# Optimization experiments

Measured on AMD Instinct MI355X. Metric: run time of the kernel, lower is better.

## Reference

```python
import jax, jax.numpy as jnp
import numpy as np

B, T, C, H = 8, 1024, 1024, 16
D = C // H
EPS = 1e-5

def _ln(x, g, b):
    mu = jnp.mean(x, axis=-1, keepdims=True)
    var = jnp.var(x, axis=-1, keepdims=True)
    return (x - mu) * jax.lax.rsqrt(var + EPS) * g + b

def _build_mask(cond_mask, cond_len, token_len):
    # Vectorized form of the per-batch Python-loop mask in the torch module.
    counts = jnp.sum(cond_mask, axis=-1)            # [B] number of valid cond tokens
    rows = jnp.arange(T)
    cols = jnp.arange(T)
    # all rows may attend to the first counts[i] (cond) columns
    m_cond = cols[None, None, :] < counts[:, None, None]          # [B,1,T]
    m_cond = jnp.broadcast_to(m_cond, (B, T, T))
    # block-causal tiled pattern on rows/cols >= cond_len:
    # value = (col - cond_len) % token_len <= (row - cond_len) % token_len
    pattern = ((cols[None, :] - cond_len) % token_len) <= ((rows[:, None] - cond_len) % token_len)
    m_block = (rows[:, None] >= cond_len) & (cols[None, :] >= cond_len) & pattern  # [T,T]
    # cols >= cond_len: overwritten by block pattern (rows < cond_len stay 0 there)
    mask = jnp.where(cols[None, None, :] < cond_len, m_cond, m_block[None, :, :])
    return mask[:, None, :, :]                      # [B,1,T,T] bool

def _attn(x, Wq, bq, Wk, bk, Wv, bv, Wp, bp, cond_mask, cond_len, token_len):
    q = (x @ Wq + bq).reshape(B, T, H, D).transpose(0, 2, 1, 3)  # [B,H,T,D]
    k = (x @ Wk + bk).reshape(B, T, H, D).transpose(0, 2, 1, 3)
    v = (x @ Wv + bv).reshape(B, T, H, D).transpose(0, 2, 1, 3)
    att = jnp.einsum('bhqd,bhkd->bhqk', q, k) * (1.0 / np.sqrt(D))
    mask = _build_mask(cond_mask, cond_len, token_len)
    att = jnp.where(mask, att, -jnp.inf)
    att = jax.nn.softmax(att, axis=-1)
    y = jnp.einsum('bhqk,bhkd->bhqd', att, v)
    y = y.transpose(0, 2, 1, 3).reshape(B, T, C)
    return y @ Wp + bp

def setup_inputs() -> dict:
    key = jax.random.key(0)
    ks = jax.random.split(key, 16)
    cond_len, token_len = 256, 768
    s = 1.0 / np.sqrt(C)
    counts = jax.random.randint(ks[0], (B,), 1, cond_len + 1)
    cond_mask = (jnp.arange(T)[None, :] < counts[:, None]).astype(jnp.int32)
    return {
        'x': jax.random.normal(ks[1], (B, T, C), jnp.float32),
        'ln1_g': jnp.ones((C,), jnp.float32), 'ln1_b': jnp.zeros((C,), jnp.float32),
        'Wq': jax.random.normal(ks[2], (C, C), jnp.float32) * s, 'bq': jnp.zeros((C,), jnp.float32),
        'Wk': jax.random.normal(ks[3], (C, C), jnp.float32) * s, 'bk': jnp.zeros((C,), jnp.float32),
        'Wv': jax.random.normal(ks[4], (C, C), jnp.float32) * s, 'bv': jnp.zeros((C,), jnp.float32),
        'Wp': jax.random.normal(ks[5], (C, C), jnp.float32) * s, 'bp': jnp.zeros((C,), jnp.float32),
        'ln2_g': jnp.ones((C,), jnp.float32), 'ln2_b': jnp.zeros((C,), jnp.float32),
        'W1': jax.random.normal(ks[6], (C, 4 * C), jnp.float32) * s, 'b1': jnp.zeros((4 * C,), jnp.float32),
        'W2': jax.random.normal(ks[7], (4 * C, C), jnp.float32) * (0.5 * s), 'b2': jnp.zeros((C,), jnp.float32),
        'cond_mask': cond_mask,
        'cond_len': cond_len,
        'token_len': token_len,
    }

def reference(x, ln1_g, ln1_b, Wq, bq, Wk, bk, Wv, bv, Wp, bp, ln2_g, ln2_b, W1, b1, W2, b2, cond_mask, cond_len, token_len):
    x = x + _attn(_ln(x, ln1_g, ln1_b), Wq, bq, Wk, bk, Wv, bv, Wp, bp, cond_mask, cond_len, token_len)
    h = _ln(x, ln2_g, ln2_b)
    x = x + (jax.nn.gelu(h @ W1 + b1, approximate=False) @ W2 + b2)
    return x
```

## Files before the change

kernel.cpp:

```cpp
#include <hip/hip_runtime.h>
#include <hip/hip_bf16.h>
#include <cstdint>
#include <cstddef>

typedef __attribute__((ext_vector_type(8))) short short8;
typedef __attribute__((ext_vector_type(4))) float f32x4;
typedef __attribute__((ext_vector_type(4))) unsigned short us4;

#define MFMA_BF16(a, b, c) __builtin_amdgcn_mfma_f32_16x16x32_bf16((a), (b), (c), 0, 0, 0)
#define VMCNT(n) asm volatile("s_waitcnt vmcnt(" #n ")" ::: "memory")

__device__ __forceinline__ unsigned short f2bf(float f) {
  unsigned int u = __float_as_uint(f);
  u += 0x7FFFu + ((u >> 16) & 1u);
  return (unsigned short)(u >> 16);
}

typedef const void __attribute__((address_space(1)))* as1_cvp;
typedef void __attribute__((address_space(3)))* as3_vp;
__device__ __forceinline__ void gll16(const short* g, short* l) {
#if defined(__HIP_DEVICE_COMPILE__)
  __builtin_amdgcn_global_load_lds((as1_cvp)g, (as3_vp)l, 16, 0, 0);
#else
  (void)g; (void)l;
#endif
}

__global__ void count_kernel(const int* __restrict__ cm, int* __restrict__ counts) {
  __shared__ int sd[256];
  const int b = blockIdx.x, t = threadIdx.x;
  int s = 0;
  for (int i = t; i < 1024; i += 256) s += cm[b * 1024 + i];
  sd[t] = s; __syncthreads();
  for (int k = 128; k > 0; k >>= 1) { if (t < k) sd[t] += sd[t + k]; __syncthreads(); }
  if (t == 0) counts[b] = sd[0];
}

__global__ void pack_bias_kernel(const float* __restrict__ bq, const float* __restrict__ bk,
                                 const float* __restrict__ bv, float* __restrict__ dst) {
  int i = blockIdx.x * 256 + threadIdx.x;
  dst[i] = (i < 1024) ? bq[i] : (i < 2048 ? bk[i - 1024] : bv[i - 2048]);
}

__global__ void transpose_kernel(const float* __restrict__ src, unsigned short* __restrict__ dst,
                                 int R, int C) {
  __shared__ float tile[32][33];
  const int c0 = blockIdx.x * 32, r0 = blockIdx.y * 32;
  const int tx = threadIdx.x, ty = threadIdx.y;
  #pragma unroll
  for (int i = ty; i < 32; i += 8)
    tile[i][tx] = src[(size_t)(r0 + i) * C + (c0 + tx)];
  __syncthreads();
  #pragma unroll
  for (int i = ty; i < 32; i += 8)
    dst[(size_t)(c0 + i) * R + (r0 + tx)] = f2bf(tile[tx][i]);
}

__global__ void vtrans_kernel(const short* __restrict__ qkv, short* __restrict__ vtr) {
  __shared__ short tile[32][33];
  const int bh = blockIdx.z;
  const int t0 = blockIdx.x * 32, d0 = blockIdx.y * 32;
  const int b = bh >> 4, h = bh & 15;
  const int tx = threadIdx.x, ty = threadIdx.y;
  const short* src = qkv + (size_t)b * 1024 * 3072 + 2048 + h * 64;
  #pragma unroll
  for (int i = ty; i < 32; i += 8)
    tile[i][tx] = src[(size_t)(t0 + i) * 3072 + d0 + tx];
  __syncthreads();
  short* dst = vtr + (size_t)bh * 65536;
  #pragma unroll
  for (int i = ty; i < 32; i += 8)
    dst[(d0 + i) * 1024 + t0 + tx] = tile[tx][i];
}

__global__ __launch_bounds__(256) void ln_kernel(const float* __restrict__ in,
                                                 const float* __restrict__ gw,
                                                 const float* __restrict__ bw,
                                                 unsigned short* __restrict__ out) {
  const int row = blockIdx.x, t = threadIdx.x;
  const float4 v = ((const float4*)(in + (size_t)row * 1024))[t];
  float s = v.x + v.y + v.z + v.w;
  float ss = v.x * v.x + v.y * v.y + v.z * v.z + v.w * v.w;
  #pragma unroll
  for (int o = 32; o >= 1; o >>= 1) { s += __shfl_down(s, o, 64); ss += __shfl_down(ss, o, 64); }
  __shared__ float red[8];
  if ((t & 63) == 0) { red[t >> 6] = s; red[4 + (t >> 6)] = ss; }
  __syncthreads();
  const float S  = red[0] + red[1] + red[2] + red[3];
  const float SS = red[4] + red[5] + red[6] + red[7];
  const float mu = S * (1.0f / 1024.0f);
  const float var = SS * (1.0f / 1024.0f) - mu * mu;
  const float rs = rsqrtf(var + 1e-5f);
  const int c = t * 4;
  const float4 g4 = ((const float4*)gw)[t];
  const float4 b4 = ((const float4*)bw)[t];
  us4 o4;
  o4[0] = f2bf((v.x - mu) * rs * g4.x + b4.x);
  o4[1] = f2bf((v.y - mu) * rs * g4.y + b4.y);
  o4[2] = f2bf((v.z - mu) * rs * g4.z + b4.z);
  o4[3] = f2bf((v.w - mu) * rs * g4.w + b4.w);
  *(us4*)(out + (size_t)row * 1024 + c) = o4;
}

template <int EPI>
__global__ __launch_bounds__(512, 1) void gemm_k2_kernel(
    const short* __restrict__ A, const short* __restrict__ BT,
    const float* __restrict__ bias, int N, int K, int gm,
    unsigned short* __restrict__ outb, float* __restrict__ outf,
    const float* __restrict__ res) {
  __shared__ alignas(16) short lds[73728];
  const int t = threadIdx.x;
  const int l = t & 63, w = t >> 6;
  const int lq = l & 15, g = l >> 4;
  const int wr = w >> 2, wc = w & 3;
  const int cpx = (int)gridDim.x >> 3;
  const int wid = ((int)blockIdx.x & 7) * cpx + ((int)blockIdx.x >> 3);
  const int bm = (wid % gm) * 256, bn = (wid / gm) * 128;
  const int NT = K >> 6;

  const int csw = ((t & 7) ^ ((t >> 3) & 7)) * 8;
  const int sA = t >> 3;
  const int sB = ((t >> 8) & 1) * 64 + ((t >> 3) & 31);

  const f32x4 z4 = {0.f, 0.f, 0.f, 0.f};
  f32x4 acc[8][2];
  #pragma unroll
  for (int i = 0; i < 8; i++) { acc[i][0] = z4; acc[i][1] = z4; }

  auto stageA = [&](int buf, int h, int k0) {
    const short* src = A + (size_t)(bm + h * 64 + sA) * K + k0 + csw;
    short* dst = lds + buf * 24576 + h * 8192 + t * 8;
    gll16(src, dst);
    gll16(src + (size_t)128 * K, dst + 4096);
  };
  auto stageB = [&](int buf, int h, int k0) {
    const short* src = BT + (size_t)(bn + h * 32 + sB) * K + k0 + csw;
    short* dst = lds + buf * 24576 + 16384 + h * 4096 + t * 8;
    gll16(src, dst);
  };
  auto rdA = [&](int buf, int mh, int mi2, int kk) {
    const int ra = wr * 64 + mi2 * 16 + lq;
    const int unit = (kk * 4 + g) ^ (ra & 7);
    return *(const short8*)(lds + buf * 24576 + mh * 8192 + ra * 64 + unit * 8);
  };
  auto rdB = [&](int buf, int ni2, int kk) {
    const int h = wc & 1;
    const int rb = (wc >> 1) * 32 + ni2 * 16 + lq;
    const int unit = (kk * 4 + g) ^ (rb & 7);
    return *(const short8*)(lds + buf * 24576 + 16384 + h * 4096 + rb * 64 + unit * 8);
  };

  stageA(0, 0, 0);  stageB(0, 0, 0);
  stageA(0, 1, 0);  stageB(0, 1, 0);
  stageA(1, 0, 64); stageB(1, 0, 64);
  VMCNT(3);
  __builtin_amdgcn_s_barrier();

  int cur = 0;
  for (int v = 0; v < NT; ++v) {
    const int nx1 = (cur == 2) ? 0 : cur + 1;
    const int nx2 = (nx1 == 2) ? 0 : nx1 + 1;
    short8 a[4][2], b[2][2], a2[4][2];
    #pragma unroll
    for (int mi2 = 0; mi2 < 4; ++mi2)
      #pragma unroll
      for (int kk = 0; kk < 2; ++kk) a[mi2][kk] = rdA(cur, 0, mi2, kk);
    #pragma unroll
    for (int ni2 = 0; ni2 < 2; ++ni2)
      #pragma unroll
      for (int kk = 0; kk < 2; ++kk) b[ni2][kk] = rdB(cur, ni2, kk);
    if (v + 1 < NT) { stageA(nx1, 1, (v + 1) * 64); stageB(nx1, 1, (v + 1) * 64); }
    __builtin_amdgcn_s_setprio(1);
    #pragma unroll
    for (int mi2 = 0; mi2 < 4; ++mi2)
      #pragma unroll
      for (int ni2 = 0; ni2 < 2; ++ni2)
        #pragma unroll
        for (int kk = 0; kk < 2; ++kk)
          acc[mi2][ni2] = MFMA_BF16(a[mi2][kk], b[ni2][kk], acc[mi2][ni2]);
    __builtin_amdgcn_s_setprio(0);
    #pragma unroll
    for (int mi2 = 0; mi2 < 4; ++mi2)
      #pragma unroll
      for (int kk = 0; kk < 2; ++kk) a2[mi2][kk] = rdA(cur, 1, mi2, kk);
    if (v + 2 < NT) {
      stageA(nx2, 0, (v + 2) * 64); stageB(nx2, 0, (v + 2) * 64);
      VMCNT(3);
    } else {
      VMCNT(0);
    }
    __builtin_amdgcn_s_barrier();
    __builtin_amdgcn_s_setprio(1);
    #pragma unroll
    for (int mi2 = 0; mi2 < 4; ++mi2)
      #pragma unroll
      for (int ni2 = 0; ni2 < 2; ++ni2)
        #pragma unroll
        for (int kk = 0; kk < 2; ++kk)
          acc[4 + mi2][ni2] = MFMA_BF16(a2[mi2][kk], b[ni2][kk], acc[4 + mi2][ni2]);
    __builtin_amdgcn_s_setprio(0);
    cur = nx1;
  }

  if (EPI == 2) {
    #pragma unroll
    for (int mi = 0; mi < 8; ++mi) {
      #pragma unroll
      for (int ni = 0; ni < 2; ++ni) {
        const int col = bn + wc * 32 + ni * 16 + lq;
        const float bv = bias[col];
        #pragma unroll
        for (int r = 0; r < 4; ++r) {
          const int row = bm + wr * 128 + (mi >> 2) * 64 + (mi & 3) * 16 + 4 * g + r;
          const size_t idx = (size_t)row * N + col;
          outf[idx] = acc[mi][ni][r] + bv + res[idx];
        }
      }
    }
    return;
  }

  unsigned short* eb = (unsigned short*)lds;
  #pragma unroll
  for (int mi = 0; mi < 8; ++mi) {
    #pragma unroll
    for (int ni = 0; ni < 2; ++ni) {
      const int col = wc * 32 + ni * 16 + lq;
      const float bv = bias[bn + col];
      #pragma unroll
      for (int r = 0; r < 4; ++r) {
        const int row = wr * 128 + (mi >> 2) * 64 + (mi & 3) * 16 + 4 * g + r;
        float vv = acc[mi][ni][r] + bv;
        if (EPI == 1) vv = 0.5f * vv * (1.0f + erff(vv * 0.70710678118654752440f));
        eb[row * 128 + col] = f2bf(vv);
      }
    }
  }
  __syncthreads();
  #pragma unroll
  for (int it = 0; it < 8; ++it) {
    const int unit = it * 512 + t;
    const int row = unit >> 4, c8 = unit & 15;
    const short8 vv = *(const short8*)(lds + unit * 8);
    *(short8*)((short*)outb + (size_t)(bm + row) * N + bn + c8 * 8) = vv;
  }
}

__global__ __launch_bounds__(64) void attn_kernel(
    const short* __restrict__ qkv, const short* __restrict__ vtr,
    unsigned short* __restrict__ y, const int* __restrict__ counts) {
  const int blk = blockIdx.x;
  const int slot = blk >> 3;
  const int p = slot & 31;
  const int bh = ((slot >> 5) << 3) | (blk & 7);
  const int b = bh >> 4, h = bh & 15;
  const int l = threadIdx.x & 63;
  const int lq = l & 15, g = l >> 4;
  const int qb0 = p * 16, qb1 = (63 - p) * 16;
  const int count = counts[b];

  const short* base  = qkv + (size_t)b * 1024 * 3072 + h * 64;
  const short* vbase = vtr + (size_t)bh * 65536;

  short8 qf[2][2];
  {
    const short* qr0 = base + (size_t)(qb0 + lq) * 3072 + 8 * g;
    const short* qr1 = base + (size_t)(qb1 + lq) * 3072 + 8 * g;
    qf[0][0] = *(const short8*)qr0; qf[0][1] = *(const short8*)(qr0 + 32);
    qf[1][0] = *(const short8*)qr1; qf[1][1] = *(const short8*)(qr1 + 32);
  }

  const f32x4 z4 = {0.f, 0.f, 0.f, 0.f};
  f32x4 oacc[2][4];
  #pragma unroll
  for (int grp = 0; grp < 2; ++grp)
    #pragma unroll
    for (int dc = 0; dc < 4; ++dc) oacc[grp][dc] = z4;
  float mrun[2] = {-1e30f, -1e30f};
  float lrun[2] = {0.f, 0.f};
  const int permrow = 8 * (lq >> 2) + (lq & 3);
  const float SC = 0.125f * 1.44269504088896f;

  const int ncond = min((count + 31) >> 5, 8);
  const int ncausal = (qb1 + 16 - 256 + 31) >> 5;
  const int nt = ncond + ncausal;
  auto kv_of = [&](int i) { return i < ncond ? i * 32 : 256 + (i - ncond) * 32; };

  auto loadt = [&](int kv0, short8 (&kr)[4], short8 (&vr)[4]) {
    const short* ka = base + (size_t)(kv0 + permrow) * 3072 + 1024 + 8 * g;
    kr[0] = *(const short8*)ka;
    kr[1] = *(const short8*)(ka + 32);
    kr[2] = *(const short8*)(ka + 4 * 3072);
    kr[3] = *(const short8*)(ka + 4 * 3072 + 32);
    #pragma unroll
    for (int dc = 0; dc < 4; ++dc)
      vr[dc] = *(const short8*)(vbase + (16 * dc + lq) * 1024 + kv0 + 8 * g);
  };

  auto compute = [&](int i, const short8 (&kr)[4], const short8 (&vr)[4]) {
    const int kv0 = kv_of(i);
    const bool isCond = (i < ncond);
    #pragma unroll
    for (int grp = 0; grp < 2; ++grp) {
      const int qb = grp ? qb1 : qb0;
      if (!isCond && kv0 >= qb + 16) continue;
      const bool needMask = isCond ? (kv0 + 32 > count) : (kv0 + 31 > qb);
      f32x4 sA = z4, sB = z4;
      __builtin_amdgcn_s_setprio(1);
      sA = MFMA_BF16(kr[0], qf[grp][0], sA);
      sA = MFMA_BF16(kr[1], qf[grp][1], sA);
      sB = MFMA_BF16(kr[2], qf[grp][0], sB);
      sB = MFMA_BF16(kr[3], qf[grp][1], sB);
      __builtin_amdgcn_s_setprio(0);
      const int q = qb + lq;
      float mx = -1e30f;
      if (needMask) {
        #pragma unroll
        for (int r = 0; r < 4; ++r) {
          const int colA = kv0 + 8 * g + r, colB = colA + 4;
          const bool okA = isCond ? (colA < count) : (colA <= q);
          const bool okB = isCond ? (colB < count) : (colB <= q);
          const float vA = okA ? sA[r] * SC : -1e30f;
          const float vB = okB ? sB[r] * SC : -1e30f;
          sA[r] = vA; sB[r] = vB;
          mx = fmaxf(fmaxf(vA, vB), mx);
        }
      } else {
        #pragma unroll
        for (int r = 0; r < 4; ++r) {
          const float vA = sA[r] * SC, vB = sB[r] * SC;
          sA[r] = vA; sB[r] = vB;
          mx = fmaxf(fmaxf(vA, vB), mx);
        }
      }
      mx = fmaxf(mx, __shfl_xor(mx, 16, 64));
      mx = fmaxf(mx, __shfl_xor(mx, 32, 64));
      float m = mrun[grp];
      if (!__all(mx <= m + 8.0f)) {
        const float mn = fmaxf(m, mx);
        const float sf = exp2f(m - mn);
        lrun[grp] *= sf;
        #pragma unroll
        for (int dc = 0; dc < 4; ++dc)
          #pragma unroll
          for (int r = 0; r < 4; ++r) oacc[grp][dc][r] *= sf;
        mrun[grp] = mn; m = mn;
      }
      float ps = 0.f;
      #pragma unroll
      for (int r = 0; r < 4; ++r) {
        const float aa = exp2f(sA[r] - m);
        const float c2 = exp2f(sB[r] - m);
        sA[r] = aa; sB[r] = c2; ps += aa + c2;
      }
      ps += __shfl_xor(ps, 16, 64);
      ps += __shfl_xor(ps, 32, 64);
      lrun[grp] += ps;
      union { short8 s8; __hip_bfloat162 h2[4]; } pu;
      pu.h2[0] = __float22bfloat162_rn(float2{sA[0], sA[1]});
      pu.h2[1] = __float22bfloat162_rn(float2{sA[2], sA[3]});
      pu.h2[2] = __float22bfloat162_rn(float2{sB[0], sB[1]});
      pu.h2[3] = __float22bfloat162_rn(float2{sB[2], sB[3]});
      __builtin_amdgcn_s_setprio(1);
      #pragma unroll
      for (int dc = 0; dc < 4; ++dc)
        oacc[grp][dc] = MFMA_BF16(vr[dc], pu.s8, oacc[grp][dc]);
      __builtin_amdgcn_s_setprio(0);
    }
  };

  short8 kb0[4], vb0[4], kb1[4], vb1[4];
  loadt(kv_of(0), kb0, vb0);
  for (int i = 0; i < nt; i += 2) {
    if (i + 1 < nt) loadt(kv_of(i + 1), kb1, vb1);
    compute(i, kb0, vb0);
    if (i + 1 >= nt) break;
    if (i + 2 < nt) loadt(kv_of(i + 2), kb0, vb0);
    compute(i + 1, kb1, vb1);
  }

  #pragma unroll
  for (int grp = 0; grp < 2; ++grp) {
    const int qb = grp ? qb1 : qb0;
    const float inv = 1.0f / lrun[grp];
    unsigned short* yr = y + (size_t)(b * 1024 + qb + lq) * 1024 + h * 64;
    #pragma unroll
    for (int dc = 0; dc < 4; ++dc)
      #pragma unroll
      for (int r = 0; r < 4; ++r)
        yr[16 * dc + 4 * g + r] = f2bf(oacc[grp][dc][r] * inv);
  }
}

extern "C" void kernel_launch(void* const* d_in, const int* in_sizes, int n_in,
                              void* d_out, int out_size, void* d_ws, size_t ws_size,
                              hipStream_t stream) {
  (void)in_sizes; (void)n_in; (void)out_size; (void)ws_size;
  const float* x     = (const float*)d_in[0];
  const float* ln1_g = (const float*)d_in[1];
  const float* ln1_b = (const float*)d_in[2];
  const float* Wq    = (const float*)d_in[3];
  const float* bq    = (const float*)d_in[4];
  const float* Wk    = (const float*)d_in[5];
  const float* bk    = (const float*)d_in[6];
  const float* Wv    = (const float*)d_in[7];
  const float* bv    = (const float*)d_in[8];
  const float* Wp    = (const float*)d_in[9];
  const float* bp    = (const float*)d_in[10];
  const float* ln2_g = (const float*)d_in[11];
  const float* ln2_b = (const float*)d_in[12];
  const float* W1    = (const float*)d_in[13];
  const float* b1    = (const float*)d_in[14];
  const float* W2    = (const float*)d_in[15];
  const float* b2    = (const float*)d_in[16];
  const int* cond_mask = (const int*)d_in[17];

  char* ws = (char*)d_ws;
  const size_t MB = 1u << 20;
  short* xn    = (short*)(ws + 0);
  short* vtr   = (short*)(ws + 0);
  short* qkv   = (short*)(ws + 16 * MB);
  short* act   = (short*)(ws + 0);
  unsigned short* yb = (unsigned short*)(ws + 64 * MB);
  float* x1    = (float*)(ws + 80 * MB);
  short* hb    = (short*)(ws + 112 * MB);
  short* wqkvT = (short*)(ws + 128 * MB);
  short* wpT   = (short*)(ws + 134 * MB);
  short* w1T   = (short*)(ws + 136 * MB);
  short* w2T   = (short*)(ws + 144 * MB);
  float* bqkv  = (float*)(ws + 152 * MB);
  int* counts  = (int*)(ws + 152 * MB + 16384);

  const dim3 tb(32, 8);
  count_kernel<<<8, 256, 0, stream>>>(cond_mask, counts);
  pack_bias_kernel<<<12, 256, 0, stream>>>(bq, bk, bv, bqkv);
  transpose_kernel<<<dim3(32, 32), tb, 0, stream>>>(Wq, (unsigned short*)wqkvT, 1024, 1024);
  transpose_kernel<<<dim3(32, 32), tb, 0, stream>>>(Wk, (unsigned short*)(wqkvT + 1024 * 1024), 1024, 1024);
  transpose_kernel<<<dim3(32, 32), tb, 0, stream>>>(Wv, (unsigned short*)(wqkvT + 2 * 1024 * 1024), 1024, 1024);
  transpose_kernel<<<dim3(32, 32), tb, 0, stream>>>(Wp, (unsigned short*)wpT, 1024, 1024);
  transpose_kernel<<<dim3(128, 32), tb, 0, stream>>>(W1, (unsigned short*)w1T, 1024, 4096);
  transpose_kernel<<<dim3(32, 128), tb, 0, stream>>>(W2, (unsigned short*)w2T, 4096, 1024);
  ln_kernel<<<8192, 256, 0, stream>>>(x, ln1_g, ln1_b, (unsigned short*)xn);

  gemm_k2_kernel<0><<<768, 512, 0, stream>>>(xn, wqkvT, bqkv, 3072, 1024, 32,
                                             (unsigned short*)qkv, nullptr, nullptr);
  vtrans_kernel<<<dim3(32, 2, 128), tb, 0, stream>>>(qkv, vtr);
  attn_kernel<<<4096, 64, 0, stream>>>(qkv, vtr, yb, counts);
  gemm_k2_kernel<2><<<256, 512, 0, stream>>>((const short*)yb, wpT, bp, 1024, 1024, 32,
                                             nullptr, x1, x);
  ln_kernel<<<8192, 256, 0, stream>>>(x1, ln2_g, ln2_b, (unsigned short*)hb);
  gemm_k2_kernel<1><<<1024, 512, 0, stream>>>(hb, w1T, b1, 4096, 1024, 32,
                                              (unsigned short*)act, nullptr, nullptr);
  gemm_k2_kernel<2><<<256, 512, 0, stream>>>(act, w2T, b2, 1024, 4096, 32,
                                             nullptr, (float*)d_out, x1);
}
```

Baseline: 471.5 us.

## Retile GEMMs to 128x256 blocks, pre-pack K/V tiles, fold softmax scale into Q

The GEMM kernel moves from 512-thread 256x128 tiles with K-step 64 to 256-thread 128x256 tiles with K-step 32, and two blocks per CU. GELU switches from erf to a tanh-style exp2 approximation. Q is pre-scaled in the QKV epilogue, and a new kvpack kernel lays out K and V tiles so attention loads are contiguous. Attention now runs four waves per block and defers the row-sum shuffle to the end. Risks are the GELU approximation error and the cost of the extra pack pass.

```diff
diff --git a/kernel.cpp b/kernel.cpp
--- a/kernel.cpp
+++ b/kernel.cpp
@@ -14,6 +14,12 @@
   unsigned int u = __float_as_uint(f);
   u += 0x7FFFu + ((u >> 16) & 1u);
   return (unsigned short)(u >> 16);
+}
+
+__device__ __forceinline__ float gelu_fast(float v) {
+  const float u = v * (0.79788456f + 0.03567741f * v * v);
+  const float e = exp2f(u * 2.88539008f);
+  return v - v * __builtin_amdgcn_rcpf(e + 1.0f);
 }
 
 typedef const void __attribute__((address_space(1)))* as1_cvp;
@@ -71,6 +77,31 @@
   #pragma unroll
   for (int i = ty; i < 32; i += 8)
     dst[(d0 + i) * 1024 + t0 + tx] = tile[tx][i];
+}
+
+__global__ __launch_bounds__(64) void kvpack_kernel(
+    const short* __restrict__ qkv, const short* __restrict__ vtr,
+    short* __restrict__ kp, short* __restrict__ vp) {
+  const int blk = blockIdx.x;
+  const int bh = blk >> 5, ti = blk & 31;
+  const int b = bh >> 4, h = bh & 15;
+  const int l = threadIdx.x & 63;
+  const int lq = l & 15, g = l >> 4;
+  const int kv0 = ti * 32;
+  const int permrow = 8 * (lq >> 2) + (lq & 3);
+  const short* ka = qkv + (size_t)b * 1024 * 3072 + h * 64
+                    + (size_t)(kv0 + permrow) * 3072 + 1024 + 8 * g;
+  short* kd = kp + (size_t)blk * 2048 + l * 8;
+  *(short8*)(kd)        = *(const short8*)ka;
+  *(short8*)(kd + 512)  = *(const short8*)(ka + 32);
+  *(short8*)(kd + 1024) = *(const short8*)(ka + 4 * 3072);
+  *(short8*)(kd + 1536) = *(const short8*)(ka + 4 * 3072 + 32);
+  const short* vb = vtr + (size_t)bh * 65536;
+  short* vd = vp + (size_t)blk * 2048 + l * 8;
+  #pragma unroll
+  for (int dc = 0; dc < 4; ++dc)
+    *(short8*)(vd + dc * 512) =
+        *(const short8*)(vb + (16 * dc + lq) * 1024 + kv0 + 8 * g);
 }
 
 __global__ __launch_bounds__(256) void ln_kernel(const float* __restrict__ in,
@@ -103,101 +134,82 @@
 }
 
 template <int EPI>
-__global__ __launch_bounds__(512, 1) void gemm_k2_kernel(
+__global__ __launch_bounds__(256, 2) void gemm128_kernel(
     const short* __restrict__ A, const short* __restrict__ BT,
     const float* __restrict__ bias, int N, int K, int gm,
     unsigned short* __restrict__ outb, float* __restrict__ outf,
     const float* __restrict__ res) {
-  __shared__ alignas(16) short lds[73728];
+  __shared__ alignas(16) short lds[36864];
   const int t = threadIdx.x;
   const int l = t & 63, w = t >> 6;
   const int lq = l & 15, g = l >> 4;
-  const int wr = w >> 2, wc = w & 3;
+  const int wc = w;
   const int cpx = (int)gridDim.x >> 3;
   const int wid = ((int)blockIdx.x & 7) * cpx + ((int)blockIdx.x >> 3);
-  const int bm = (wid % gm) * 256, bn = (wid / gm) * 128;
-  const int NT = K >> 6;
-
-  const int csw = ((t & 7) ^ ((t >> 3) & 7)) * 8;
-  const int sA = t >> 3;
-  const int sB = ((t >> 8) & 1) * 64 + ((t >> 3) & 31);
+  const int bm = (wid % gm) * 128, bn = (wid / gm) * 256;
+  const int NT = K >> 5;
+
+  const int csw = ((t & 3) ^ ((t >> 3) & 3)) * 8;
+  const int sr = t >> 2;
 
   const f32x4 z4 = {0.f, 0.f, 0.f, 0.f};
-  f32x4 acc[8][2];
-  #pragma unroll
-  for (int i = 0; i < 8; i++) { acc[i][0] = z4; acc[i][1] = z4; }
-
-  auto stageA = [&](int buf, int h, int k0) {
-    const short* src = A + (size_t)(bm + h * 64 + sA) * K + k0 + csw;
-    short* dst = lds + buf * 24576 + h * 8192 + t * 8;
+  f32x4 acc[8][4];
+  #pragma unroll
+  for (int i = 0; i < 8; i++)
+    #pragma unroll
+    for (int j = 0; j < 4; j++) acc[i][j] = z4;
+
+  auto stageA = [&](int buf, int k0) {
+    const short* src = A + (size_t)(bm + sr) * K + k0 + csw;
+    short* dst = lds + buf * 12288 + t * 8;
     gll16(src, dst);
+    gll16(src + (size_t)64 * K, dst + 2048);
+  };
+  auto stageB = [&](int buf, int k0) {
+    const short* src = BT + (size_t)(bn + sr) * K + k0 + csw;
+    short* dst = lds + buf * 12288 + 4096 + t * 8;
+    gll16(src, dst);
+    gll16(src + (size_t)64 * K,  dst + 2048);
     gll16(src + (size_t)128 * K, dst + 4096);
-  };
-  auto stageB = [&](int buf, int h, int k0) {
-    const short* src = BT + (size_t)(bn + h * 32 + sB) * K + k0 + csw;
-    short* dst = lds + buf * 24576 + 16384 + h * 4096 + t * 8;
-    gll16(src, dst);
-  };
-  auto rdA = [&](int buf, int mh, int mi2, int kk) {
-    const int ra = wr * 64 + mi2 * 16 + lq;
-    const int unit = (kk * 4 + g) ^ (ra & 7);
-    return *(const short8*)(lds + buf * 24576 + mh * 8192 + ra * 64 + unit * 8);
-  };
-  auto rdB = [&](int buf, int ni2, int kk) {
-    const int h = wc & 1;
-    const int rb = (wc >> 1) * 32 + ni2 * 16 + lq;
-    const int unit = (kk * 4 + g) ^ (rb & 7);
-    return *(const short8*)(lds + buf * 24576 + 16384 + h * 4096 + rb * 64 + unit * 8);
-  };
-
-  stageA(0, 0, 0);  stageB(0, 0, 0);
-  stageA(0, 1, 0);  stageB(0, 1, 0);
-  stageA(1, 0, 64); stageB(1, 0, 64);
-  VMCNT(3);
+    gll16(src + (size_t)192 * K, dst + 6144);
+  };
+  const int swu = (g ^ ((lq >> 1) & 3)) * 8;
+  auto rdA = [&](int buf, int mi) {
+    const int ra = mi * 16 + lq;
+    return *(const short8*)(lds + buf * 12288 + ra * 32 + swu);
+  };
+  auto rdB = [&](int buf, int ni) {
+    const int rb = wc * 64 + ni * 16 + lq;
+    return *(const short8*)(lds + buf * 12288 + 4096 + rb * 32 + swu);
+  };
+
+  stageA(0, 0);  stageB(0, 0);
+  stageA(1, 32); stageB(1, 32);
+  VMCNT(6);
   __builtin_amdgcn_s_barrier();
 
   int cur = 0;
   for (int v = 0; v < NT; ++v) {
     const int nx1 = (cur == 2) ? 0 : cur + 1;
     const int nx2 = (nx1 == 2) ? 0 : nx1 + 1;
-    short8 a[4][2], b[2][2], a2[4][2];
-    #pragma unroll
-    for (int mi2 = 0; mi2 < 4; ++mi2)
-      #pragma unroll
-      for (int kk = 0; kk < 2; ++kk) a[mi2][kk] = rdA(cur, 0, mi2, kk);
-    #pragma unroll
-    for (int ni2 = 0; ni2 < 2; ++ni2)
-      #pragma unroll
-      for (int kk = 0; kk < 2; ++kk) b[ni2][kk] = rdB(cur, ni2, kk);
-    if (v + 1 < NT) { stageA(nx1, 1, (v + 1) * 64); stageB(nx1, 1, (v + 1) * 64); }
-    __builtin_amdgcn_s_setprio(1);
-    #pragma unroll
-    for (int mi2 = 0; mi2 < 4; ++mi2)
-      #pragma unroll
-      for (int ni2 = 0; ni2 < 2; ++ni2)
-        #pragma unroll
-        for (int kk = 0; kk < 2; ++kk)
-          acc[mi2][ni2] = MFMA_BF16(a[mi2][kk], b[ni2][kk], acc[mi2][ni2]);
-    __builtin_amdgcn_s_setprio(0);
-    #pragma unroll
-    for (int mi2 = 0; mi2 < 4; ++mi2)
-      #pragma unroll
-      for (int kk = 0; kk < 2; ++kk) a2[mi2][kk] = rdA(cur, 1, mi2, kk);
+    short8 a[8], b[4];
+    #pragma unroll
+    for (int mi = 0; mi < 8; ++mi) a[mi] = rdA(cur, mi);
+    #pragma unroll
+    for (int ni = 0; ni < 4; ++ni) b[ni] = rdB(cur, ni);
     if (v + 2 < NT) {
-      stageA(nx2, 0, (v + 2) * 64); stageB(nx2, 0, (v + 2) * 64);
-      VMCNT(3);
+      stageA(nx2, (v + 2) * 32); stageB(nx2, (v + 2) * 32);
+      VMCNT(6);
     } else {
       VMCNT(0);
     }
     __builtin_amdgcn_s_barrier();
     __builtin_amdgcn_s_setprio(1);
     #pragma unroll
-    for (int mi2 = 0; mi2 < 4; ++mi2)
-      #pragma unroll
-      for (int ni2 = 0; ni2 < 2; ++ni2)
-        #pragma unroll
-        for (int kk = 0; kk < 2; ++kk)
-          acc[4 + mi2][ni2] = MFMA_BF16(a2[mi2][kk], b[ni2][kk], acc[4 + mi2][ni2]);
+    for (int mi = 0; mi < 8; ++mi)
+      #pragma unroll
+      for (int ni = 0; ni < 4; ++ni)
+        acc[mi][ni] = MFMA_BF16(a[mi], b[ni], acc[mi][ni]);
     __builtin_amdgcn_s_setprio(0);
     cur = nx1;
   }
@@ -206,12 +218,12 @@
     #pragma unroll
     for (int mi = 0; mi < 8; ++mi) {
       #pragma unroll
-      for (int ni = 0; ni < 2; ++ni) {
-        const int col = bn + wc * 32 + ni * 16 + lq;
+      for (int ni = 0; ni < 4; ++ni) {
+        const int col = bn + wc * 64 + ni * 16 + lq;
         const float bv = bias[col];
         #pragma unroll
         for (int r = 0; r < 4; ++r) {
-          const int row = bm + wr * 128 + (mi >> 2) * 64 + (mi & 3) * 16 + 4 * g + r;
+          const int row = bm + mi * 16 + 4 * g + r;
           const size_t idx = (size_t)row * N + col;
           outf[idx] = acc[mi][ni][r] + bv + res[idx];
         }
@@ -220,47 +232,53 @@
     return;
   }
 
+  __syncthreads();
+  const float qscale = (EPI == 3 && bn < 1024) ? 0.125f * 1.44269504088896f : 1.0f;
   unsigned short* eb = (unsigned short*)lds;
   #pragma unroll
   for (int mi = 0; mi < 8; ++mi) {
     #pragma unroll
-    for (int ni = 0; ni < 2; ++ni) {
-      const int col = wc * 32 + ni * 16 + lq;
+    for (int ni = 0; ni < 4; ++ni) {
+      const int col = wc * 64 + ni * 16 + lq;
       const float bv = bias[bn + col];
       #pragma unroll
       for (int r = 0; r < 4; ++r) {
-        const int row = wr * 128 + (mi >> 2) * 64 + (mi & 3) * 16 + 4 * g + r;
+        const int row = mi * 16 + 4 * g + r;
         float vv = acc[mi][ni][r] + bv;
-        if (EPI == 1) vv = 0.5f * vv * (1.0f + erff(vv * 0.70710678118654752440f));
-        eb[row * 128 + col] = f2bf(vv);
+        if (EPI == 1) vv = gelu_fast(vv);
+        if (EPI == 3) vv *= qscale;
+        eb[row * 256 + col] = f2bf(vv);
       }
     }
   }
   __syncthreads();
   #pragma unroll
-  for (int it = 0; it < 8; ++it) {
-    const int unit = it * 512 + t;
-    const int row = unit >> 4, c8 = unit & 15;
+  for (int it = 0; it < 16; ++it) {
+    const int unit = it * 256 + t;
+    const int row = unit >> 5, c8 = unit & 31;
     const short8 vv = *(const short8*)(lds + unit * 8);
     *(short8*)((short*)outb + (size_t)(bm + row) * N + bn + c8 * 8) = vv;
   }
 }
 
-__global__ __launch_bounds__(64) void attn_kernel(
-    const short* __restrict__ qkv, const short* __restrict__ vtr,
-    unsigned short* __restrict__ y, const int* __restrict__ counts) {
+__global__ __launch_bounds__(256) void attn_kernel(
+    const short* __restrict__ qkv, const short* __restrict__ kp,
+    const short* __restrict__ vp, unsigned short* __restrict__ y,
+    const int* __restrict__ counts) {
   const int blk = blockIdx.x;
   const int slot = blk >> 3;
-  const int p = slot & 31;
-  const int bh = ((slot >> 5) << 3) | (blk & 7);
+  const int pb = slot & 7;
+  const int bh = ((slot >> 3) << 3) | (blk & 7);
   const int b = bh >> 4, h = bh & 15;
-  const int l = threadIdx.x & 63;
+  const int w = threadIdx.x >> 6, l = threadIdx.x & 63;
+  const int p = pb + 8 * w;
   const int lq = l & 15, g = l >> 4;
   const int qb0 = p * 16, qb1 = (63 - p) * 16;
   const int count = counts[b];
 
   const short* base  = qkv + (size_t)b * 1024 * 3072 + h * 64;
-  const short* vbase = vtr + (size_t)bh * 65536;
+  const short* kbase = kp + (size_t)bh * 65536 + l * 8;
+  const short* vbase = vp + (size_t)bh * 65536 + l * 8;
 
   short8 qf[2][2];
   {
@@ -278,23 +296,21 @@
     for (int dc = 0; dc < 4; ++dc) oacc[grp][dc] = z4;
   float mrun[2] = {-1e30f, -1e30f};
   float lrun[2] = {0.f, 0.f};
-  const int permrow = 8 * (lq >> 2) + (lq & 3);
-  const float SC = 0.125f * 1.44269504088896f;
-
   const int ncond = min((count + 31) >> 5, 8);
   const int ncausal = (qb1 + 16 - 256 + 31) >> 5;
   const int nt = ncond + ncausal;
   auto kv_of = [&](int i) { return i < ncond ? i * 32 : 256 + (i - ncond) * 32; };
 
   auto loadt = [&](int kv0, short8 (&kr)[4], short8 (&vr)[4]) {
-    const short* ka = base + (size_t)(kv0 + permrow) * 3072 + 1024 + 8 * g;
-    kr[0] = *(const short8*)ka;
-    kr[1] = *(const short8*)(ka + 32);
-    kr[2] = *(const short8*)(ka + 4 * 3072);
-    kr[3] = *(const short8*)(ka + 4 * 3072 + 32);
+    const short* kpp = kbase + (size_t)(kv0 >> 5) * 2048;
+    kr[0] = *(const short8*)kpp;
+    kr[1] = *(const short8*)(kpp + 512);
+    kr[2] = *(const short8*)(kpp + 1024);
+    kr[3] = *(const short8*)(kpp + 1536);
+    const short* vpp = vbase + (size_t)(kv0 >> 5) * 2048;
     #pragma unroll
     for (int dc = 0; dc < 4; ++dc)
-      vr[dc] = *(const short8*)(vbase + (16 * dc + lq) * 1024 + kv0 + 8 * g);
+      vr[dc] = *(const short8*)(vpp + dc * 512);
   };
 
   auto compute = [&](int i, const short8 (&kr)[4], const short8 (&vr)[4]) {
@@ -320,18 +336,15 @@
           const int colA = kv0 + 8 * g + r, colB = colA + 4;
           const bool okA = isCond ? (colA < count) : (colA <= q);
           const bool okB = isCond ? (colB < count) : (colB <= q);
-          const float vA = okA ? sA[r] * SC : -1e30f;
-          const float vB = okB ? sB[r] * SC : -1e30f;
+          const float vA = okA ? sA[r] : -1e30f;
+          const float vB = okB ? sB[r] : -1e30f;
           sA[r] = vA; sB[r] = vB;
           mx = fmaxf(fmaxf(vA, vB), mx);
         }
       } else {
         #pragma unroll
-        for (int r = 0; r < 4; ++r) {
-          const float vA = sA[r] * SC, vB = sB[r] * SC;
-          sA[r] = vA; sB[r] = vB;
-          mx = fmaxf(fmaxf(vA, vB), mx);
-        }
+        for (int r = 0; r < 4; ++r)
+          mx = fmaxf(fmaxf(sA[r], sB[r]), mx);
       }
       mx = fmaxf(mx, __shfl_xor(mx, 16, 64));
       mx = fmaxf(mx, __shfl_xor(mx, 32, 64));
@@ -353,8 +366,6 @@
         const float c2 = exp2f(sB[r] - m);
         sA[r] = aa; sB[r] = c2; ps += aa + c2;
       }
-      ps += __shfl_xor(ps, 16, 64);
-      ps += __shfl_xor(ps, 32, 64);
       lrun[grp] += ps;
       union { short8 s8; __hip_bfloat162 h2[4]; } pu;
       pu.h2[0] = __float22bfloat162_rn(float2{sA[0], sA[1]});
@@ -381,8 +392,11 @@
 
   #pragma unroll
   for (int grp = 0; grp < 2; ++grp) {
+    float ls = lrun[grp];
+    ls += __shfl_xor(ls, 16, 64);
+    ls += __shfl_xor(ls, 32, 64);
+    const float inv = 1.0f / ls;
     const int qb = grp ? qb1 : qb0;
-    const float inv = 1.0f / lrun[grp];
     unsigned short* yr = y + (size_t)(b * 1024 + qb + lq) * 1024 + h * 64;
     #pragma unroll
     for (int dc = 0; dc < 4; ++dc)
@@ -418,11 +432,13 @@
   char* ws = (char*)d_ws;
   const size_t MB = 1u << 20;
   short* xn    = (short*)(ws + 0);
-  short* vtr   = (short*)(ws + 0);
+  short* kpack = (short*)(ws + 0);
   short* qkv   = (short*)(ws + 16 * MB);
   short* act   = (short*)(ws + 0);
   unsigned short* yb = (unsigned short*)(ws + 64 * MB);
+  short* vtr   = (short*)(ws + 80 * MB);
   float* x1    = (float*)(ws + 80 * MB);
+  short* vpack = (short*)(ws + 112 * MB);
   short* hb    = (short*)(ws + 112 * MB);
   short* wqkvT = (short*)(ws + 128 * MB);
   short* wpT   = (short*)(ws + 134 * MB);
@@ -442,15 +458,16 @@
   transpose_kernel<<<dim3(32, 128), tb, 0, stream>>>(W2, (unsigned short*)w2T, 4096, 1024);
   ln_kernel<<<8192, 256, 0, stream>>>(x, ln1_g, ln1_b, (unsigned short*)xn);
 
-  gemm_k2_kernel<0><<<768, 512, 0, stream>>>(xn, wqkvT, bqkv, 3072, 1024, 32,
+  gemm128_kernel<3><<<768, 256, 0, stream>>>(xn, wqkvT, bqkv, 3072, 1024, 64,
                                              (unsigned short*)qkv, nullptr, nullptr);
   vtrans_kernel<<<dim3(32, 2, 128), tb, 0, stream>>>(qkv, vtr);
-  attn_kernel<<<4096, 64, 0, stream>>>(qkv, vtr, yb, counts);
-  gemm_k2_kernel<2><<<256, 512, 0, stream>>>((const short*)yb, wpT, bp, 1024, 1024, 32,
+  kvpack_kernel<<<4096, 64, 0, stream>>>(qkv, vtr, kpack, vpack);
+  attn_kernel<<<1024, 256, 0, stream>>>(qkv, kpack, vpack, yb, counts);
+  gemm128_kernel<2><<<256, 256, 0, stream>>>((const short*)yb, wpT, bp, 1024, 1024, 64,
                                              nullptr, x1, x);
   ln_kernel<<<8192, 256, 0, stream>>>(x1, ln2_g, ln2_b, (unsigned short*)hb);
-  gemm_k2_kernel<1><<<1024, 512, 0, stream>>>(hb, w1T, b1, 4096, 1024, 32,
+  gemm128_kernel<1><<<1024, 256, 0, stream>>>(hb, w1T, b1, 4096, 1024, 64,
                                               (unsigned short*)act, nullptr, nullptr);
-  gemm_k2_kernel<2><<<256, 512, 0, stream>>>(act, w2T, b2, 1024, 4096, 32,
+  gemm128_kernel<2><<<256, 256, 0, stream>>>(act, w2T, b2, 1024, 4096, 64,
                                              nullptr, (float*)d_out, x1);
 }
```

Result: faster. 409.6 us (-13.1%).
